# Performance work log

Measured on AMD Instinct MI355X. Metric: run time of the kernel, lower is better.

Reference implementation:

```python
import jax, jax.numpy as jnp
import numpy as np
from jax import lax

B, T, P, H, O = 64, 96, 256, 128, 24  # batch, seq_len, num_points, hidden_dim, pred_len


def setup_inputs() -> dict:
    key = jax.random.key(0)
    ks = jax.random.split(key, 7)
    s = 1.0 / np.sqrt(H)  # torch LSTM/Linear default init scale
    return {
        "x": jax.random.normal(ks[0], (B, T, P, 1), dtype=jnp.float32),
        "W_ih": jax.random.uniform(ks[1], (P, 4 * H, 1), jnp.float32, -s, s),
        "W_hh": jax.random.uniform(ks[2], (P, 4 * H, H), jnp.float32, -s, s),
        "b_ih": jax.random.uniform(ks[3], (P, 4 * H), jnp.float32, -s, s),
        "b_hh": jax.random.uniform(ks[4], (P, 4 * H), jnp.float32, -s, s),
        "W_fc": jax.random.uniform(ks[5], (P, O, H), jnp.float32, -s, s),
        "b_fc": jax.random.uniform(ks[6], (P, O), jnp.float32, -s, s),
    }


def reference(x, W_ih, W_hh, b_ih, b_hh, W_fc, b_fc):
    # x: [B, T, P, F]; model uses only feature 0
    xs = x[..., 0]  # [B, T, P]
    # input_dim == 1, so input-to-gate contribution is a scaled broadcast of W_ih
    # precompute for all timesteps: [T, B, P, 4H]
    gx = jnp.einsum("btp,pg->tbpg", xs, W_ih[:, :, 0]) + (b_ih + b_hh)

    def step(carry, gxt):
        h, c = carry  # [B, P, H] each
        gates = gxt + jnp.einsum("bph,pgh->bpg", h, W_hh)  # [B, P, 4H]
        i, f, g, o = jnp.split(gates, 4, axis=-1)  # torch gate order i,f,g,o
        i = jax.nn.sigmoid(i)
        f = jax.nn.sigmoid(f)
        g = jnp.tanh(g)
        o = jax.nn.sigmoid(o)
        c = f * c + i * g
        h = o * jnp.tanh(c)
        return (h, c), None

    h0 = jnp.zeros((B, P, H), dtype=x.dtype)
    (h, _), _ = lax.scan(step, (h0, h0), gx)
    # per-point Linear on final hidden state: [B, P, O]
    out = jnp.einsum("bph,poh->bpo", h, W_fc) + b_fc
    # original stacks point outputs on last dim -> [B, pred_len, P]
    return jnp.transpose(out, (0, 2, 1))
```

## Files before the change

### kernel.cpp

```cpp
#include <hip/hip_runtime.h>
#include <hip/hip_bf16.h>

#define Bdim 64
#define Tdim 96
#define Pdim 256
#define Hdim 128
#define Gdim 512
#define Odim 24
#define WROW 132

typedef __bf16 bf16x8 __attribute__((ext_vector_type(8)));
typedef float  f32x16 __attribute__((ext_vector_type(16)));

union BF8 { uint2 u2[2]; unsigned short s[8]; bf16x8 v; };

__device__ __forceinline__ unsigned short f2bf(float f) {
    unsigned int u = __float_as_uint(f);
    u = (u + 0x7FFFu + ((u >> 16) & 1u)) >> 16;
    return (unsigned short)u;
}
__device__ __forceinline__ float bf2f(unsigned short s) {
    return __uint_as_float(((unsigned int)s) << 16);
}
__device__ __forceinline__ float sigm(float x) {
    return __builtin_amdgcn_rcpf(1.0f + __expf(-x));
}
__device__ __forceinline__ float tanh_fast(float x) {
    return __builtin_fmaf(2.0f, sigm(2.0f * x), -1.0f);
}

__global__ __launch_bounds__(512, 2)
void lstm_fused(const float* __restrict__ x,
                const float* __restrict__ W_ih,
                const float* __restrict__ W_hh,
                const float* __restrict__ b_ih,
                const float* __restrict__ b_hh,
                const float* __restrict__ W_fc,
                const float* __restrict__ b_fc,
                float* __restrict__ out)
{
    __shared__ unsigned short hlds[Bdim * WROW];
    __shared__ float wihl[Gdim];
    __shared__ float gbl[Gdim];

    const int p   = blockIdx.x;
    const int tid = threadIdx.x;
    const int w   = tid >> 6;
    const int l   = tid & 63;
    const int l31 = l & 31;
    const int hi  = l >> 5;

    {
        int r = tid;
        int orow = ((r & 3) << 7) | (r >> 2);
        wihl[r] = W_ih[(size_t)p * Gdim + orow];
        gbl[r]  = b_ih[(size_t)p * Gdim + orow] + b_hh[(size_t)p * Gdim + orow];
    }
    for (int i = tid; i < Bdim * WROW; i += 512) hlds[i] = 0;

    bf16x8 afr[2][8];
    {
        const float* wp = W_hh + (size_t)p * Gdim * Hdim;
        #pragma unroll
        for (int mt = 0; mt < 2; ++mt) {
            int m = w * 64 + mt * 32 + l31;
            int orow = ((m & 3) << 7) | (m >> 2);
            const float* rowp = wp + orow * Hdim;
            #pragma unroll
            for (int ks = 0; ks < 8; ++ks) {
                int k0 = ks * 16 + hi * 8;
                float4 va = *(const float4*)(rowp + k0);
                float4 vb = *(const float4*)(rowp + k0 + 4);
                BF8 u;
                u.s[0] = f2bf(va.x); u.s[1] = f2bf(va.y);
                u.s[2] = f2bf(va.z); u.s[3] = f2bf(va.w);
                u.s[4] = f2bf(vb.x); u.s[5] = f2bf(vb.y);
                u.s[6] = f2bf(vb.z); u.s[7] = f2bf(vb.w);
                afr[mt][ks] = u.v;
            }
        }
    }

    __syncthreads();

    float wihr[2][16], gbr[2][16];
    #pragma unroll
    for (int mt = 0; mt < 2; ++mt)
        #pragma unroll
        for (int j = 0; j < 16; ++j) {
            int rp = w * 64 + mt * 32 + (j & 3) + ((j >> 2) << 3) + (hi << 2);
            wihr[mt][j] = wihl[rp];
            gbr[mt][j]  = gbl[rp];
        }

    float cre[2][2][4];
    #pragma unroll
    for (int mt = 0; mt < 2; ++mt)
        for (int nt = 0; nt < 2; ++nt)
            for (int q = 0; q < 4; ++q) cre[mt][nt][q] = 0.f;

    const float* xp = x + p;
    float xv0 = xp[(size_t)(l31 * Tdim) * Pdim];
    float xv1 = xp[(size_t)((l31 + 32) * Tdim) * Pdim];

    for (int t = 0; t < Tdim; ++t) {
        float xn0 = 0.f, xn1 = 0.f;
        if (t + 1 < Tdim) {
            xn0 = xp[(size_t)(l31 * Tdim + t + 1) * Pdim];
            xn1 = xp[(size_t)((l31 + 32) * Tdim + t + 1) * Pdim];
        }

        f32x16 acc[2][2];
        #pragma unroll
        for (int mt = 0; mt < 2; ++mt)
            #pragma unroll
            for (int j = 0; j < 16; ++j) {
                acc[mt][0][j] = __builtin_fmaf(xv0, wihr[mt][j], gbr[mt][j]);
                acc[mt][1][j] = __builtin_fmaf(xv1, wihr[mt][j], gbr[mt][j]);
            }

        #pragma unroll
        for (int ks = 0; ks < 8; ++ks) {
            int boff = ks * 32 + hi * 16;
            BF8 b0, b1;
            const char* hbase = (const char*)hlds;
            b0.u2[0] = *(const uint2*)(hbase + l31 * (WROW * 2) + boff);
            b0.u2[1] = *(const uint2*)(hbase + l31 * (WROW * 2) + boff + 8);
            b1.u2[0] = *(const uint2*)(hbase + (l31 + 32) * (WROW * 2) + boff);
            b1.u2[1] = *(const uint2*)(hbase + (l31 + 32) * (WROW * 2) + boff + 8);
            acc[0][0] = __builtin_amdgcn_mfma_f32_32x32x16_bf16(afr[0][ks], b0.v, acc[0][0], 0, 0, 0);
            acc[0][1] = __builtin_amdgcn_mfma_f32_32x32x16_bf16(afr[0][ks], b1.v, acc[0][1], 0, 0, 0);
            acc[1][0] = __builtin_amdgcn_mfma_f32_32x32x16_bf16(afr[1][ks], b0.v, acc[1][0], 0, 0, 0);
            acc[1][1] = __builtin_amdgcn_mfma_f32_32x32x16_bf16(afr[1][ks], b1.v, acc[1][1], 0, 0, 0);
        }

        __syncthreads();

        #pragma unroll
        for (int mt = 0; mt < 2; ++mt)
            #pragma unroll
            for (int nt = 0; nt < 2; ++nt)
                #pragma unroll
                for (int q = 0; q < 4; ++q) {
                    float iv = sigm(acc[mt][nt][4 * q + 0]);
                    float fv = sigm(acc[mt][nt][4 * q + 1]);
                    float gv = tanh_fast(acc[mt][nt][4 * q + 2]);
                    float ov = sigm(acc[mt][nt][4 * q + 3]);
                    float c  = __builtin_fmaf(fv, cre[mt][nt][q], iv * gv);
                    cre[mt][nt][q] = c;
                    float hv = ov * tanh_fast(c);
                    int k = w * 16 + mt * 8 + q * 2 + hi;
                    int b = nt * 32 + l31;
                    hlds[b * WROW + k] = f2bf(hv);
                }

        __syncthreads();
        xv0 = xn0; xv1 = xn1;
    }

    const float* wfc = W_fc + (size_t)p * Odim * Hdim;
    const float* bfc = b_fc + (size_t)p * Odim;
    for (int i = tid; i < Bdim * Odim; i += 512) {
        int o = i % Odim;
        int b = i / Odim;
        float s = bfc[o];
        const float* wr = wfc + o * Hdim;
        const unsigned short* hr = hlds + b * WROW;
        #pragma unroll 8
        for (int k2 = 0; k2 < Hdim; ++k2)
            s = __builtin_fmaf(wr[k2], bf2f(hr[k2]), s);
        out[(size_t)b * Odim * Pdim + (size_t)o * Pdim + p] = s;
    }
}

extern "C" void kernel_launch(void* const* d_in, const int* in_sizes, int n_in,
                              void* d_out, int out_size, void* d_ws, size_t ws_size,
                              hipStream_t stream) {
    const float* x    = (const float*)d_in[0];
    const float* W_ih = (const float*)d_in[1];
    const float* W_hh = (const float*)d_in[2];
    const float* b_ih = (const float*)d_in[3];
    const float* b_hh = (const float*)d_in[4];
    const float* W_fc = (const float*)d_in[5];
    const float* b_fc = (const float*)d_in[6];
    float* out = (float*)d_out;

    lstm_fused<<<dim3(Pdim), dim3(512), 0, stream>>>(x, W_ih, W_hh, b_ih, b_hh, W_fc, b_fc, out);
}
```

Before: 453.3 us.

## Double-buffer hidden state, use 1024 threads, fold input/bias into MFMA

Doubles the block to 1024 threads so each wave computes one 32-row gate tile instead of two. The hidden-state buffer is double-buffered, which removes one of the two barriers per timestep. The input term and biases are folded into an extra MFMA k-slice, replacing the per-timestep FMA initialisation, and log2(e) is pre-scaled into the weights so activations use exp2 directly. The extra bf16 rounding of x, bias and pre-scaled weights slightly changes numerics, and the larger block raises register pressure per wave.

Result: faster. 400.9 us (-11.6%).

```diff
diff --git a/kernel.cpp b/kernel.cpp
--- a/kernel.cpp
+++ b/kernel.cpp
@@ -22,14 +22,18 @@
 __device__ __forceinline__ float bf2f(unsigned short s) {
     return __uint_as_float(((unsigned int)s) << 16);
 }
-__device__ __forceinline__ float sigm(float x) {
-    return __builtin_amdgcn_rcpf(1.0f + __expf(-x));
+__device__ __forceinline__ float exp2_fast(float x) {
+#if __has_builtin(__builtin_amdgcn_exp2f)
+    return __builtin_amdgcn_exp2f(x);
+#else
+    return __expf(x * 0.6931471805599453f);
+#endif
 }
-__device__ __forceinline__ float tanh_fast(float x) {
-    return __builtin_fmaf(2.0f, sigm(2.0f * x), -1.0f);
+__device__ __forceinline__ float sigm2(float y) {
+    return __builtin_amdgcn_rcpf(1.0f + exp2_fast(-y));
 }
 
-__global__ __launch_bounds__(512, 2)
+__global__ __launch_bounds__(1024, 4)
 void lstm_fused(const float* __restrict__ x,
                 const float* __restrict__ W_ih,
                 const float* __restrict__ W_hh,
@@ -39,9 +43,7 @@
                 const float* __restrict__ b_fc,
                 float* __restrict__ out)
 {
-    __shared__ unsigned short hlds[Bdim * WROW];
-    __shared__ float wihl[Gdim];
-    __shared__ float gbl[Gdim];
+    __shared__ unsigned short hl[2][Bdim * WROW];
 
     const int p   = blockIdx.x;
     const int tid = threadIdx.x;
@@ -50,59 +52,52 @@
     const int l31 = l & 31;
     const int hi  = l >> 5;
 
+    const float L1 = 1.4426950408889634f;
+
+    for (int i = tid; i < 2 * Bdim * WROW; i += 1024) ((unsigned short*)hl)[i] = 0;
+
+    bf16x8 afr[9];
     {
-        int r = tid;
-        int orow = ((r & 3) << 7) | (r >> 2);
-        wihl[r] = W_ih[(size_t)p * Gdim + orow];
-        gbl[r]  = b_ih[(size_t)p * Gdim + orow] + b_hh[(size_t)p * Gdim + orow];
-    }
-    for (int i = tid; i < Bdim * WROW; i += 512) hlds[i] = 0;
-
-    bf16x8 afr[2][8];
-    {
-        const float* wp = W_hh + (size_t)p * Gdim * Hdim;
+        const int rp   = w * 32 + l31;
+        const int orow = ((rp & 3) << 7) | (rp >> 2);
+        const float sc = ((rp & 3) == 2) ? (2.0f * L1) : L1;
+        const float* rowp = W_hh + (size_t)p * Gdim * Hdim + (size_t)orow * Hdim;
         #pragma unroll
-        for (int mt = 0; mt < 2; ++mt) {
-            int m = w * 64 + mt * 32 + l31;
-            int orow = ((m & 3) << 7) | (m >> 2);
-            const float* rowp = wp + orow * Hdim;
-            #pragma unroll
-            for (int ks = 0; ks < 8; ++ks) {
-                int k0 = ks * 16 + hi * 8;
-                float4 va = *(const float4*)(rowp + k0);
-                float4 vb = *(const float4*)(rowp + k0 + 4);
-                BF8 u;
-                u.s[0] = f2bf(va.x); u.s[1] = f2bf(va.y);
-                u.s[2] = f2bf(va.z); u.s[3] = f2bf(va.w);
-                u.s[4] = f2bf(vb.x); u.s[5] = f2bf(vb.y);
-                u.s[6] = f2bf(vb.z); u.s[7] = f2bf(vb.w);
-                afr[mt][ks] = u.v;
-            }
+        for (int ks = 0; ks < 8; ++ks) {
+            int k0 = ks * 16 + hi * 8;
+            float4 va = *(const float4*)(rowp + k0);
+            float4 vb = *(const float4*)(rowp + k0 + 4);
+            BF8 u;
+            u.s[0] = f2bf(sc * va.x); u.s[1] = f2bf(sc * va.y);
+            u.s[2] = f2bf(sc * va.z); u.s[3] = f2bf(sc * va.w);
+            u.s[4] = f2bf(sc * vb.x); u.s[5] = f2bf(sc * vb.y);
+            u.s[6] = f2bf(sc * vb.z); u.s[7] = f2bf(sc * vb.w);
+            afr[ks] = u.v;
         }
+        BF8 u9;
+        #pragma unroll
+        for (int j = 0; j < 8; ++j) u9.s[j] = 0;
+        if (hi == 0) {
+            u9.s[0] = f2bf(sc * W_ih[(size_t)p * Gdim + orow]);
+            u9.s[1] = f2bf(sc * (b_ih[(size_t)p * Gdim + orow] +
+                                 b_hh[(size_t)p * Gdim + orow]));
+        }
+        afr[8] = u9.v;
     }
 
-    __syncthreads();
-
-    float wihr[2][16], gbr[2][16];
+    float cre[2][4];
     #pragma unroll
-    for (int mt = 0; mt < 2; ++mt)
+    for (int nt = 0; nt < 2; ++nt)
         #pragma unroll
-        for (int j = 0; j < 16; ++j) {
-            int rp = w * 64 + mt * 32 + (j & 3) + ((j >> 2) << 3) + (hi << 2);
-            wihr[mt][j] = wihl[rp];
-            gbr[mt][j]  = gbl[rp];
-        }
-
-    float cre[2][2][4];
-    #pragma unroll
-    for (int mt = 0; mt < 2; ++mt)
-        for (int nt = 0; nt < 2; ++nt)
-            for (int q = 0; q < 4; ++q) cre[mt][nt][q] = 0.f;
+        for (int q = 0; q < 4; ++q) cre[nt][q] = 0.f;
 
     const float* xp = x + p;
     float xv0 = xp[(size_t)(l31 * Tdim) * Pdim];
     float xv1 = xp[(size_t)((l31 + 32) * Tdim) * Pdim];
 
+    __syncthreads();
+
+    int cur = 0;
     for (int t = 0; t < Tdim; ++t) {
         float xn0 = 0.f, xn1 = 0.f;
         if (t + 1 < Tdim) {
@@ -110,62 +105,70 @@
             xn1 = xp[(size_t)((l31 + 32) * Tdim + t + 1) * Pdim];
         }
 
-        f32x16 acc[2][2];
+        f32x16 acc[2];
         #pragma unroll
-        for (int mt = 0; mt < 2; ++mt)
-            #pragma unroll
-            for (int j = 0; j < 16; ++j) {
-                acc[mt][0][j] = __builtin_fmaf(xv0, wihr[mt][j], gbr[mt][j]);
-                acc[mt][1][j] = __builtin_fmaf(xv1, wihr[mt][j], gbr[mt][j]);
-            }
+        for (int j = 0; j < 16; ++j) { acc[0][j] = 0.f; acc[1][j] = 0.f; }
 
+        const char* hbase = (const char*)hl[cur];
         #pragma unroll
         for (int ks = 0; ks < 8; ++ks) {
             int boff = ks * 32 + hi * 16;
             BF8 b0, b1;
-            const char* hbase = (const char*)hlds;
             b0.u2[0] = *(const uint2*)(hbase + l31 * (WROW * 2) + boff);
             b0.u2[1] = *(const uint2*)(hbase + l31 * (WROW * 2) + boff + 8);
             b1.u2[0] = *(const uint2*)(hbase + (l31 + 32) * (WROW * 2) + boff);
             b1.u2[1] = *(const uint2*)(hbase + (l31 + 32) * (WROW * 2) + boff + 8);
-            acc[0][0] = __builtin_amdgcn_mfma_f32_32x32x16_bf16(afr[0][ks], b0.v, acc[0][0], 0, 0, 0);
-            acc[0][1] = __builtin_amdgcn_mfma_f32_32x32x16_bf16(afr[0][ks], b1.v, acc[0][1], 0, 0, 0);
-            acc[1][0] = __builtin_amdgcn_mfma_f32_32x32x16_bf16(afr[1][ks], b0.v, acc[1][0], 0, 0, 0);
-            acc[1][1] = __builtin_amdgcn_mfma_f32_32x32x16_bf16(afr[1][ks], b1.v, acc[1][1], 0, 0, 0);
+            acc[0] = __builtin_amdgcn_mfma_f32_32x32x16_bf16(afr[ks], b0.v, acc[0], 0, 0, 0);
+            acc[1] = __builtin_amdgcn_mfma_f32_32x32x16_bf16(afr[ks], b1.v, acc[1], 0, 0, 0);
+        }
+        {
+            BF8 b0, b1;
+            #pragma unroll
+            for (int j = 0; j < 8; ++j) { b0.s[j] = 0; b1.s[j] = 0; }
+            unsigned short onebf = hi ? (unsigned short)0 : (unsigned short)0x3F80;
+            b0.s[0] = hi ? (unsigned short)0 : f2bf(xv0);
+            b0.s[1] = onebf;
+            b1.s[0] = hi ? (unsigned short)0 : f2bf(xv1);
+            b1.s[1] = onebf;
+            acc[0] = __builtin_amdgcn_mfma_f32_32x32x16_bf16(afr[8], b0.v, acc[0], 0, 0, 0);
+            acc[1] = __builtin_amdgcn_mfma_f32_32x32x16_bf16(afr[8], b1.v, acc[1], 0, 0, 0);
+        }
+
+        unsigned short* hw = hl[cur ^ 1];
+        #pragma unroll
+        for (int nt = 0; nt < 2; ++nt) {
+            #pragma unroll
+            for (int q = 0; q < 4; ++q) {
+                float iv = sigm2(acc[nt][4 * q + 0]);
+                float fv = sigm2(acc[nt][4 * q + 1]);
+                float ug = sigm2(acc[nt][4 * q + 2]);
+                float gp = __builtin_fmaf(4.0f * L1, ug, -2.0f * L1);
+                float ov = sigm2(acc[nt][4 * q + 3]);
+                float c  = __builtin_fmaf(fv, cre[nt][q], iv * gp);
+                cre[nt][q] = c;
+                float v  = __builtin_amdgcn_rcpf(1.0f + exp2_fast(-c));
+                float th = __builtin_fmaf(2.0f, v, -1.0f);
+                float hv = ov * th;
+                int k = w * 8 + 2 * q + hi;
+                int b = l31 + 32 * nt;
+                hw[b * WROW + k] = f2bf(hv);
+            }
         }
 
         __syncthreads();
-
-        #pragma unroll
-        for (int mt = 0; mt < 2; ++mt)
-            #pragma unroll
-            for (int nt = 0; nt < 2; ++nt)
-                #pragma unroll
-                for (int q = 0; q < 4; ++q) {
-                    float iv = sigm(acc[mt][nt][4 * q + 0]);
-                    float fv = sigm(acc[mt][nt][4 * q + 1]);
-                    float gv = tanh_fast(acc[mt][nt][4 * q + 2]);
-                    float ov = sigm(acc[mt][nt][4 * q + 3]);
-                    float c  = __builtin_fmaf(fv, cre[mt][nt][q], iv * gv);
-                    cre[mt][nt][q] = c;
-                    float hv = ov * tanh_fast(c);
-                    int k = w * 16 + mt * 8 + q * 2 + hi;
-                    int b = nt * 32 + l31;
-                    hlds[b * WROW + k] = f2bf(hv);
-                }
-
-        __syncthreads();
+        cur ^= 1;
         xv0 = xn0; xv1 = xn1;
     }
 
     const float* wfc = W_fc + (size_t)p * Odim * Hdim;
     const float* bfc = b_fc + (size_t)p * Odim;
-    for (int i = tid; i < Bdim * Odim; i += 512) {
+    const unsigned short* hf = hl[cur];
+    for (int i = tid; i < Bdim * Odim; i += 1024) {
         int o = i % Odim;
         int b = i / Odim;
         float s = bfc[o];
         const float* wr = wfc + o * Hdim;
-        const unsigned short* hr = hlds + b * WROW;
+        const unsigned short* hr = hf + b * WROW;
         #pragma unroll 8
         for (int k2 = 0; k2 < Hdim; ++k2)
             s = __builtin_fmaf(wr[k2], bf2f(hr[k2]), s);
@@ -185,5 +188,5 @@
     const float* b_fc = (const float*)d_in[6];
     float* out = (float*)d_out;
 
-    lstm_fused<<<dim3(Pdim), dim3(512), 0, stream>>>(x, W_ih, W_hh, b_ih, b_hh, W_fc, b_fc, out);
+    lstm_fused<<<dim3(Pdim), dim3(1024), 0, stream>>>(x, W_ih, W_hh, b_ih, b_hh, W_fc, b_fc, out);
 }
```
